# Kernel optimization log

Measured on AMD Instinct MI355X. Metric: run time of the kernel, lower is better.

Reference implementation:

```python
import jax, jax.numpy as jnp
import numpy as np
import math

B, S, D, H, F, L, V = 16, 256, 1024, 16, 4096, 6, 32
HD = D // H
EPS = 1e-6
DIST_DECAY = 0.05  # grid-distance attention decay strength
NEG = -1e9


def _ln(x, w, b):
    mu = jnp.mean(x, axis=-1, keepdims=True)
    var = jnp.mean(jnp.square(x - mu), axis=-1, keepdims=True)
    return (x - mu) * jax.lax.rsqrt(var + EPS) * w + b


def _branch_bias():
    # branch 0: grid-distance decay (distance_matrix = |i-j|)
    # branch 1: register-flow edges i<->i+1 (chain mask)
    # branch 2: entanglement edges on even pairs (2k, 2k+1)
    # branch 3: semantic (full attention, no bias)
    i = jnp.arange(S)
    dist = jnp.abs(i[:, None] - i[None, :]).astype(jnp.float32)  # [S,S]
    reg = dist <= 1.0
    ent = (i[:, None] // 2) == (i[None, :] // 2)
    bias = jnp.stack([
        -DIST_DECAY * dist,
        jnp.where(reg, 0.0, NEG),
        jnp.where(ent, 0.0, NEG),
        jnp.zeros((S, S), jnp.float32),
    ])  # [4,S,S]
    return bias[:, None, None]  # [4,1,1,S,S]


def setup_inputs() -> dict:
    key = jax.random.key(0)
    ks = jax.random.split(key, 20)
    sd = 0.02
    inp = {
        'x': jax.random.normal(ks[0], (B, S, D), jnp.float32),
        't_emb': jax.random.normal(ks[1], (B, D), jnp.float32),
        'ln1_w': jnp.ones((L, D)), 'ln1_b': jnp.zeros((L, D)),
        'ln2_w': jnp.ones((L, D)), 'ln2_b': jnp.zeros((L, D)),
        'Wqkv': jax.random.normal(ks[2], (L, 4, D, 3 * D)) * sd,
        'Wo':   jax.random.normal(ks[3], (L, 4, D, D)) * sd,
        'Wf':   jax.random.normal(ks[4], (L, 4 * D, D)) * sd,
        'bf':   jnp.zeros((L, D)),
        'W1':   jax.random.normal(ks[5], (L, D, F)) * sd,
        'W3':   jax.random.normal(ks[6], (L, D, F)) * sd,
        'W2':   jax.random.normal(ks[7], (L, F, D)) * sd,
        'Wa':   jax.random.normal(ks[8], (L, D, 6 * D)) * sd,
        'ba':   jnp.zeros((L, 6 * D)),
        'fn_w': jnp.ones((D,)), 'fn_b': jnp.zeros((D,)),
        'Wp':   jax.random.normal(ks[9], (D, V)) * sd,
        'bp':   jnp.zeros((V,)),
    }
    return inp


def _quantum_attention(xn, Wqkv_l, Wo_l, Wf_l, bf_l, bias):
    # four attention branches computed in one batched einsum over branch axis x
    qkv = jnp.einsum('bsd,xde->xbse', xn, Wqkv_l)            # [4,B,S,3D]
    qkv = qkv.reshape(4, B, S, 3, H, HD)
    q, k, v = (jnp.moveaxis(qkv[:, :, :, j], 3, 2) for j in range(3))  # [4,B,H,S,HD]
    scores = jnp.einsum('xbhsd,xbhtd->xbhst', q, k) / math.sqrt(HD) + bias
    attn = jax.nn.softmax(scores, axis=-1)
    ctx = jnp.einsum('xbhst,xbhtd->xbhsd', attn, v)          # [4,B,H,S,HD]
    ctx = jnp.moveaxis(ctx, 2, 3).reshape(4, B, S, D)
    outs = jnp.einsum('xbsd,xde->xbse', ctx, Wo_l)           # [4,B,S,D]
    cat = jnp.moveaxis(outs, 0, 2).reshape(B, S, 4 * D)
    return cat @ Wf_l + bf_l                                  # fusion network


def reference(x, t_emb, ln1_w, ln1_b, ln2_w, ln2_b, Wqkv, Wo, Wf, bf, W1, W3, W2, Wa, ba, fn_w, fn_b, Wp, bp):
    bias = _branch_bias()
    for l in range(L):
        # AdaLN timestep conditioning: SiLU -> Linear -> chunk(6)
        a = jax.nn.silu(t_emb) @ Wa[l] + ba[l]
        sh_msa, sc_msa, g_msa, sh_mlp, sc_mlp, g_mlp = jnp.split(a, 6, axis=-1)
        xn = _ln(x, ln1_w[l], ln1_b[l])
        xn = xn * (1.0 + sc_msa[:, None]) + sh_msa[:, None]
        attn_out = _quantum_attention(xn, Wqkv[l], Wo[l], Wf[l], bf[l], bias)
        x = x + g_msa[:, None] * attn_out
        xn = _ln(x, ln2_w[l], ln2_b[l])
        xn = xn * (1.0 + sc_mlp[:, None]) + sh_mlp[:, None]
        ffn = (jax.nn.silu(xn @ W1[l]) * (xn @ W3[l])) @ W2[l]  # SwiGLU
        x = x + g_mlp[:, None] * ffn
    x = _ln(x, fn_w, fn_b)
    return x @ Wp + bp  # noise predictor logits [B,S,V]
```

## Files before the change

kernel.cpp:

```cpp
#include <hip/hip_runtime.h>
#include <hip/hip_bf16.h>
#include <math.h>

#define BB 16
#define SS 256
#define DD 1024
#define HH 16
#define HDD 64
#define FF 4096
#define LL 6
#define VV 32
#define MM (BB*SS)

using bf16 = __hip_bfloat16;
using short8 = __attribute__((ext_vector_type(8))) short;
using f32x4  = __attribute__((ext_vector_type(4))) float;

__device__ __forceinline__ float bf2f(short u){
  unsigned int x = ((unsigned int)(unsigned short)u) << 16;
  return __builtin_bit_cast(float, x);
}
__device__ __forceinline__ short f2bf(float f){
  return __builtin_bit_cast(short, __float2bfloat16(f));
}

__device__ __forceinline__ void gll16(const void* g, void* l) {
  __builtin_amdgcn_global_load_lds(
      (const __attribute__((address_space(1))) void*)g,
      (__attribute__((address_space(3))) void*)l,
      16, 0, 0);
}

__device__ __forceinline__ f32x4 mfma16(short8 a, short8 b, f32x4 c){
  return __builtin_amdgcn_mfma_f32_16x16x32_bf16(a, b, c, 0, 0, 0);
}

__device__ __forceinline__ void st_out(float* p, float v){ *p = v; }
__device__ __forceinline__ void st_out(bf16* p, float v){ *p = __float2bfloat16(v); }

__global__ __launch_bounds__(256)
void tcvt64(const float* __restrict__ in, bf16* __restrict__ out,
            int R, int C, long izs, long ozs)
{
  in  += (long)blockIdx.z * izs;
  out += (long)blockIdx.z * ozs;
  __shared__ float tl[64][65];
  int c0 = blockIdx.x * 64, r0 = blockIdx.y * 64;
  int t = threadIdx.x;
  int tr = t >> 4, tc = (t & 15) * 4;
  #pragma unroll
  for (int i = 0; i < 4; ++i) {
    f32x4 v = *(const f32x4*)(in + (long)(r0 + tr + i*16) * C + c0 + tc);
    tl[tr + i*16][tc+0] = v[0];
    tl[tr + i*16][tc+1] = v[1];
    tl[tr + i*16][tc+2] = v[2];
    tl[tr + i*16][tc+3] = v[3];
  }
  __syncthreads();
  int oc = t >> 2, rch = (t & 3) * 16;
  short8 o0, o1;
  #pragma unroll
  for (int j = 0; j < 8; ++j) o0[j] = f2bf(tl[rch + j][oc]);
  #pragma unroll
  for (int j = 0; j < 8; ++j) o1[j] = f2bf(tl[rch + 8 + j][oc]);
  *(short8*)(out + (long)(c0 + oc) * R + r0 + rch)     = o0;
  *(short8*)(out + (long)(c0 + oc) * R + r0 + rch + 8) = o1;
}

__global__ __launch_bounds__(256)
void cvt(const float* __restrict__ in, bf16* __restrict__ out)
{
  long base = ((long)blockIdx.x * 256 + threadIdx.x) * 8;
  f32x4 a = *(const f32x4*)(in + base);
  f32x4 b = *(const f32x4*)(in + base + 4);
  short8 o;
  #pragma unroll
  for (int j = 0; j < 4; ++j) { o[j] = f2bf(a[j]); o[4+j] = f2bf(b[j]); }
  *(short8*)(out + base) = o;
}

template<typename OUT>
__global__ __launch_bounds__(512, 2)
void gemm256(const bf16* __restrict__ A, const bf16* __restrict__ Bt,
             OUT* __restrict__ C, int K,
             int lda, int ldb, int ldc, int swz)
{
  __shared__ short lds[65536];
  char* L = (char*)lds;
  int lin = blockIdx.x + gridDim.x * blockIdx.y;
  if (swz) {
    int nwg = gridDim.x * gridDim.y;
    int q = nwg >> 3, r = nwg & 7;
    int xcd = lin & 7, o = lin >> 3;
    lin = (xcd < r ? xcd*(q+1) : r*(q+1) + (xcd-r)*q) + o;
  }
  const int n0 = (lin % gridDim.x) * 256;
  const int m0 = (lin / gridDim.x) * 256;
  const int t = threadIdx.x;
  const int wid = t >> 6, lane = t & 63, lo = lane & 15, hi = lane >> 4;
  const int wr = wid >> 2, wc = wid & 3;
  const int rst = t >> 3;
  const int glog = (t & 7) ^ (rst & 7);
  const int wub = wid * 1024;
  const bf16* Ap = A + (long)m0 * lda + glog * 8;
  const bf16* Bp = Bt + (long)n0 * ldb + glog * 8;
  f32x4 acc[8][4] = {};
  const int nkt = K >> 6;

  auto STAGE = [&](int kt, int p, int d) {
    const long ko = (long)kt * 64;
    char* base = L + d*65536;
    if (p < 2) {
      gll16(Ap + (long)((p*2  )*64 + rst)*lda + ko, base + (p*2  )*8192 + wub);
      gll16(Ap + (long)((p*2+1)*64 + rst)*lda + ko, base + (p*2+1)*8192 + wub);
    } else {
      int pp = p - 2;
      gll16(Bp + (long)((pp*2  )*64 + rst)*ldb + ko, base + 32768 + (pp*2  )*8192 + wub);
      gll16(Bp + (long)((pp*2+1)*64 + rst)*ldb + ko, base + 32768 + (pp*2+1)*8192 + wub);
    }
  };

  #pragma unroll
  for (int p = 0; p < 4; ++p) STAGE(0, p, 0);

  short8 af[4][2], b0[2][2], b1[2][2];
  const int gk0 = ((0*4 + hi) ^ (lo & 7)) << 4;
  const int gk1 = ((1*4 + hi) ^ (lo & 7)) << 4;

  for (int kt = 0; kt < nkt; ++kt) {
    const int d = kt & 1;
    const int ktn = (kt+1 < nkt) ? kt+1 : kt;
    char* Ab = L + d*65536;
    char* Bb = Ab + 32768;
    STAGE(ktn, 0, d^1);
    __builtin_amdgcn_sched_barrier(0);
    asm volatile("s_waitcnt vmcnt(2)" ::: "memory");
    __builtin_amdgcn_sched_barrier(0);
    __builtin_amdgcn_s_barrier();
    __builtin_amdgcn_sched_barrier(0);
    #pragma unroll
    for (int mi = 0; mi < 4; ++mi) {
      int r = wr*128 + mi*16 + lo;
      af[mi][0] = *(const short8*)(Ab + r*128 + gk0);
      af[mi][1] = *(const short8*)(Ab + r*128 + gk1);
    }
    #pragma unroll
    for (int ni = 0; ni < 2; ++ni) {
      int r = wc*64 + ni*16 + lo;
      b0[ni][0] = *(const short8*)(Bb + r*128 + gk0);
      b0[ni][1] = *(const short8*)(Bb + r*128 + gk1);
    }
    __builtin_amdgcn_s_barrier();
    __builtin_amdgcn_s_setprio(1);
    #pragma unroll
    for (int mi = 0; mi < 4; ++mi)
      #pragma unroll
      for (int ni = 0; ni < 2; ++ni) {
        acc[mi][ni] = mfma16(af[mi][0], b0[ni][0], acc[mi][ni]);
        acc[mi][ni] = mfma16(af[mi][1], b0[ni][1], acc[mi][ni]);
      }
    __builtin_amdgcn_s_setprio(0);
    __builtin_amdgcn_sched_barrier(0);
    __builtin_amdgcn_s_barrier();
    STAGE(ktn, 1, d^1);
    #pragma unroll
    for (int ni = 0; ni < 2; ++ni) {
      int r = wc*64 + (2+ni)*16 + lo;
      b1[ni][0] = *(const short8*)(Bb + r*128 + gk0);
      b1[ni][1] = *(const short8*)(Bb + r*128 + gk1);
    }
    __builtin_amdgcn_s_barrier();
    __builtin_amdgcn_s_setprio(1);
    #pragma unroll
    for (int mi = 0; mi < 4; ++mi)
      #pragma unroll
      for (int ni = 0; ni < 2; ++ni) {
        acc[mi][2+ni] = mfma16(af[mi][0], b1[ni][0], acc[mi][2+ni]);
        acc[mi][2+ni] = mfma16(af[mi][1], b1[ni][1], acc[mi][2+ni]);
      }
    __builtin_amdgcn_s_setprio(0);
    __builtin_amdgcn_sched_barrier(0);
    __builtin_amdgcn_s_barrier();
    STAGE(ktn, 2, d^1);
    #pragma unroll
    for (int mi = 0; mi < 4; ++mi) {
      int r = wr*128 + (4+mi)*16 + lo;
      af[mi][0] = *(const short8*)(Ab + r*128 + gk0);
      af[mi][1] = *(const short8*)(Ab + r*128 + gk1);
    }
    __builtin_amdgcn_s_barrier();
    __builtin_amdgcn_s_setprio(1);
    #pragma unroll
    for (int mi = 0; mi < 4; ++mi)
      #pragma unroll
      for (int ni = 0; ni < 2; ++ni) {
        acc[4+mi][2+ni] = mfma16(af[mi][0], b1[ni][0], acc[4+mi][2+ni]);
        acc[4+mi][2+ni] = mfma16(af[mi][1], b1[ni][1], acc[4+mi][2+ni]);
      }
    __builtin_amdgcn_s_setprio(0);
    __builtin_amdgcn_sched_barrier(0);
    __builtin_amdgcn_s_barrier();
    STAGE(ktn, 3, d^1);
    __builtin_amdgcn_s_barrier();
    __builtin_amdgcn_s_setprio(1);
    #pragma unroll
    for (int mi = 0; mi < 4; ++mi)
      #pragma unroll
      for (int ni = 0; ni < 2; ++ni) {
        acc[4+mi][ni] = mfma16(af[mi][0], b0[ni][0], acc[4+mi][ni]);
        acc[4+mi][ni] = mfma16(af[mi][1], b0[ni][1], acc[4+mi][ni]);
      }
    __builtin_amdgcn_s_setprio(0);
    __builtin_amdgcn_sched_barrier(0);
    __builtin_amdgcn_s_barrier();
  }
  #pragma unroll
  for (int mi = 0; mi < 8; ++mi)
    #pragma unroll
    for (int ni = 0; ni < 4; ++ni)
      #pragma unroll
      for (int r = 0; r < 4; ++r) {
        int row = m0 + wr*128 + mi*16 + hi*4 + r;
        int col = n0 + wc*64 + ni*16 + lo;
        st_out(C + (long)row * ldc + col, acc[mi][ni][r]);
      }
}

template<typename OUT>
__global__ __launch_bounds__(256)
void gemm_bt(const bf16* __restrict__ A, const bf16* __restrict__ Bt,
             OUT* __restrict__ C, int M, int N, int K,
             int lda, int ldb, int ldc,
             long azs, long bzs, long czs, int swz)
{
  const int z = blockIdx.z;
  A  += (long)z * azs;
  Bt += (long)z * bzs;
  C  += (long)z * czs;
  int bx = blockIdx.x, by = blockIdx.y;
  if (swz) {
    int nwg = gridDim.x * gridDim.y;
    int lin = bx + gridDim.x * by;
    int lin2 = (lin & 7) * (nwg >> 3) + (lin >> 3);
    bx = lin2 % gridDim.x;
    by = lin2 / gridDim.x;
  }
  const int n0 = bx * 128;
  const int m0 = by * 128;
  __shared__ short As[128*64];
  __shared__ short Bs[128*64];
  char* AsB = (char*)As;
  char* BsB = (char*)Bs;
  const int t = threadIdx.x;
  const int wid = t >> 6, lane = t & 63, lo = lane & 15, hi = lane >> 4;
  const int wr = wid >> 1, wc = wid & 1;
  const int rst  = t >> 3;
  const int glog = (t & 7) ^ (rst & 7);
  const int ldsbase = wid * 1024;
  f32x4 acc[4][4] = {};
  const bf16* Ap = A + (long)m0 * lda + glog * 8;
  const bf16* Bp = Bt + (long)n0 * ldb + glog * 8;
  const int nkt = K >> 6;
  for (int kt = 0; kt < nkt; ++kt) {
    const long ko = (long)kt * 64;
    #pragma unroll
    for (int i = 0; i < 4; ++i)
      gll16(Ap + (long)(i*32 + rst) * lda + ko, AsB + i*4096 + ldsbase);
    #pragma unroll
    for (int i = 0; i < 4; ++i)
      gll16(Bp + (long)(i*32 + rst) * ldb + ko, BsB + i*4096 + ldsbase);
    __syncthreads();
    #pragma unroll
    for (int kk = 0; kk < 2; ++kk) {
      const int g = ((kk*4 + hi) ^ (lo & 7)) << 4;
      short8 af[4], bfv[4];
      #pragma unroll
      for (int mi = 0; mi < 4; ++mi) {
        int r = wr*64 + mi*16 + lo;
        af[mi] = *(const short8*)(AsB + r*128 + g);
      }
      #pragma unroll
      for (int ni = 0; ni < 4; ++ni) {
        int r = wc*64 + ni*16 + lo;
        bfv[ni] = *(const short8*)(BsB + r*128 + g);
      }
      #pragma unroll
      for (int mi = 0; mi < 4; ++mi)
        #pragma unroll
        for (int ni = 0; ni < 4; ++ni)
          acc[mi][ni] = mfma16(af[mi], bfv[ni], acc[mi][ni]);
    }
    __syncthreads();
  }
  #pragma unroll
  for (int mi = 0; mi < 4; ++mi)
    #pragma unroll
    for (int ni = 0; ni < 4; ++ni)
      #pragma unroll
      for (int r = 0; r < 4; ++r) {
        int row = m0 + wr*64 + mi*16 + hi*4 + r;
        int col = n0 + wc*64 + ni*16 + lo;
        st_out(C + (long)row * ldc + col, acc[mi][ni][r]);
      }
}

__global__ __launch_bounds__(256)
void vtk(const bf16* __restrict__ qkv, bf16* __restrict__ vt)
{
  int xbh = blockIdx.y;
  int xc = xbh >> 8, b = (xbh >> 4) & 15, h = xbh & 15;
  int x = xc * 3;
  int tch = blockIdx.x;
  const unsigned short* src = (const unsigned short*)qkv
      + (long)(b*SS + tch*64) * 12288 + x*3072 + 2048 + h*64;
  unsigned short* dst = (unsigned short*)vt + (long)xbh * 64 * 256 + tch*64;
  __shared__ unsigned short tl[64][66];
  int t = threadIdx.x;
  #pragma unroll
  for (int i = 0; i < 16; ++i) {
    int idx = t + i*256; int tt = idx >> 6, dd = idx & 63;
    tl[tt][dd] = src[(long)tt * 12288 + dd];
  }
  __syncthreads();
  #pragma unroll
  for (int i = 0; i < 16; ++i) {
    int idx = t + i*256; int dd = idx >> 6, t2 = idx & 63;
    dst[(long)dd * 256 + t2] = tl[t2][dd];
  }
}

__device__ __forceinline__ float bias_f(int x, int i, int j){
  if (x == 0) { int d = i > j ? i - j : j - i; return -0.05f * (float)d; }
  return 0.f;
}

__global__ __launch_bounds__(256)
void attn_k(const bf16* __restrict__ qkv, const bf16* __restrict__ vt,
            bf16* __restrict__ ctx)
{
  const int xc = blockIdx.y;
  const int x = xc * 3;
  const int bh = blockIdx.x;
  const int b = bh >> 4, h = bh & 15;
  const int t = threadIdx.x, wid = t >> 6, lane = t & 63;
  const int lo = lane & 15, hi = lane >> 4;
  const int q0 = wid * 64;
  __shared__ short Pl[4][64*64];
  char* P = (char*)Pl[wid];
  const bf16* qb = qkv + (long)(b*SS) * 12288 + x*3072 + h*64;
  const bf16* kb = qb + 1024;
  const bf16* vb = vt + (long)(xc*256 + b*16 + h) * 64 * 256;

  short8 qf[4][2];
  #pragma unroll
  for (int mi = 0; mi < 4; ++mi)
    #pragma unroll
    for (int kk = 0; kk < 2; ++kk)
      qf[mi][kk] = *(const short8*)(qb + (long)(q0 + mi*16 + lo) * 12288 + kk*32 + hi*8);

  float mr[4][4], sr[4][4];
  f32x4 aco[4][4] = {};
  #pragma unroll
  for (int i = 0; i < 4; ++i)
    #pragma unroll
    for (int r = 0; r < 4; ++r) { mr[i][r] = -INFINITY; sr[i][r] = 0.f; }

  for (int c = 0; c < 4; ++c) {
    f32x4 acc[4][4] = {};
    #pragma unroll
    for (int kk = 0; kk < 2; ++kk) {
      short8 bfv[4];
      #pragma unroll
      for (int ni = 0; ni < 4; ++ni)
        bfv[ni] = *(const short8*)(kb + (long)(c*64 + ni*16 + lo) * 12288 + kk*32 + hi*8);
      #pragma unroll
      for (int mi = 0; mi < 4; ++mi)
        #pragma unroll
        for (int ni = 0; ni < 4; ++ni)
          acc[mi][ni] = mfma16(qf[mi][kk], bfv[ni], acc[mi][ni]);
    }
    float cmax[4][4];
    #pragma unroll
    for (int mi = 0; mi < 4; ++mi)
      #pragma unroll
      for (int r = 0; r < 4; ++r) cmax[mi][r] = -INFINITY;
    #pragma unroll
    for (int mi = 0; mi < 4; ++mi)
      #pragma unroll
      for (int ni = 0; ni < 4; ++ni)
        #pragma unroll
        for (int r = 0; r < 4; ++r) {
          int qq = q0 + mi*16 + hi*4 + r;
          int tt = c*64 + ni*16 + lo;
          float v = acc[mi][ni][r] * 0.125f + bias_f(x, qq, tt);
          acc[mi][ni][r] = v;
          cmax[mi][r] = fmaxf(cmax[mi][r], v);
        }
    #pragma unroll
    for (int mi = 0; mi < 4; ++mi)
      #pragma unroll
      for (int r = 0; r < 4; ++r) {
        float m = cmax[mi][r];
        #pragma unroll
        for (int d = 1; d < 16; d <<= 1) m = fmaxf(m, __shfl_xor(m, d));
        cmax[mi][r] = m;
      }
    float fs[4][4];
    #pragma unroll
    for (int mi = 0; mi < 4; ++mi)
      #pragma unroll
      for (int r = 0; r < 4; ++r) {
        float mo = mr[mi][r];
        float mn = fmaxf(mo, cmax[mi][r]);
        float f = __expf(mo - mn);
        mr[mi][r] = mn; sr[mi][r] *= f; fs[mi][r] = f;
      }
    #pragma unroll
    for (int mi = 0; mi < 4; ++mi)
      #pragma unroll
      for (int di = 0; di < 4; ++di)
        #pragma unroll
        for (int r = 0; r < 4; ++r) aco[mi][di][r] *= fs[mi][r];
    #pragma unroll
    for (int mi = 0; mi < 4; ++mi)
      #pragma unroll
      for (int ni = 0; ni < 4; ++ni)
        #pragma unroll
        for (int r = 0; r < 4; ++r) {
          int qq = mi*16 + hi*4 + r;
          float pv = __expf(acc[mi][ni][r] - mr[mi][r]);
          sr[mi][r] += pv;
          int tt = ni*16 + lo;
          int gph = ((tt >> 3) ^ (qq & 7)) << 4;
          *(bf16*)(P + qq*128 + gph + (tt & 7)*2) = __float2bfloat16(pv);
        }
    #pragma unroll
    for (int kk = 0; kk < 2; ++kk) {
      short8 pf[4], vf[4];
      #pragma unroll
      for (int mi = 0; mi < 4; ++mi) {
        int qq = mi*16 + lo;
        int gph = ((kk*4 + hi) ^ (qq & 7)) << 4;
        pf[mi] = *(const short8*)(P + qq*128 + gph);
      }
      #pragma unroll
      for (int di = 0; di < 4; ++di)
        vf[di] = *(const short8*)(vb + (long)(di*16 + lo) * 256 + c*64 + kk*32 + hi*8);
      #pragma unroll
      for (int mi = 0; mi < 4; ++mi)
        #pragma unroll
        for (int di = 0; di < 4; ++di)
          aco[mi][di] = mfma16(pf[mi], vf[di], aco[mi][di]);
    }
  }
  #pragma unroll
  for (int mi = 0; mi < 4; ++mi)
    #pragma unroll
    for (int r = 0; r < 4; ++r) {
      float s = sr[mi][r];
      #pragma unroll
      for (int d = 1; d < 16; d <<= 1) s += __shfl_xor(s, d);
      sr[mi][r] = s;
    }
  bf16* cb = ctx + (long)(b*SS) * 4096 + x*1024 + h*64;
  #pragma unroll
  for (int mi = 0; mi < 4; ++mi)
    #pragma unroll
    for (int di = 0; di < 4; ++di)
      #pragma unroll
      for (int r = 0; r < 4; ++r) {
        int row = q0 + mi*16 + hi*4 + r;
        int col = di*16 + lo;
        cb[(long)row * 4096 + col] = __float2bfloat16(aco[mi][di][r] / sr[mi][r]);
      }
}

__global__ __launch_bounds__(256)
void br12_k(const bf16* __restrict__ qkv, bf16* __restrict__ ctx)
{
  const unsigned short* Q = (const unsigned short*)qkv;
  const int wid = threadIdx.x >> 6, lane = threadIdx.x & 63;
  const int b = blockIdx.x >> 6, c = blockIdx.x & 63;
  const int i = c*4 + wid;
  const long rowQ = (long)(b*SS + i) * 12288;
  const long rb = (long)(b*SS) * 12288;
  const int jm = i > 0 ? i-1 : 0;
  const int jp = i < SS-1 ? i+1 : SS-1;
  const int j0 = i & ~1, j1 = j0 | 1;
  unsigned short* outp = (unsigned short*)ctx + (long)(b*SS + i) * 4096;
  for (int h = 0; h < HH; ++h) {
    const int off1 = 3072 + h*64 + lane;
    const int off2 = 6144 + h*64 + lane;
    float q1d = bf2f(Q[rowQ + off1]);
    float q2d = bf2f(Q[rowQ + off2]);
    float km = bf2f(Q[rb + (long)jm*12288 + off1 + 1024]);
    float k0 = bf2f(Q[rb + (long)i *12288 + off1 + 1024]);
    float kp = bf2f(Q[rb + (long)jp*12288 + off1 + 1024]);
    float ka = bf2f(Q[rb + (long)j0*12288 + off2 + 1024]);
    float kb_ = bf2f(Q[rb + (long)j1*12288 + off2 + 1024]);
    float s0 = q1d*km, s1 = q1d*k0, s2 = q1d*kp, s3 = q2d*ka, s4 = q2d*kb_;
    #pragma unroll
    for (int st = 1; st < 64; st <<= 1) {
      s0 += __shfl_xor(s0, st); s1 += __shfl_xor(s1, st); s2 += __shfl_xor(s2, st);
      s3 += __shfl_xor(s3, st); s4 += __shfl_xor(s4, st);
    }
    float lm = s0*0.125f + (i > 0      ? 0.f : -1e30f);
    float l0 = s1*0.125f;
    float lp = s2*0.125f + (i < SS-1   ? 0.f : -1e30f);
    float m1 = fmaxf(l0, fmaxf(lm, lp));
    float pm = __expf(lm-m1), p0 = __expf(l0-m1), pp = __expf(lp-m1);
    float vm = bf2f(Q[rb + (long)jm*12288 + off1 + 2048]);
    float v0 = bf2f(Q[rb + (long)i *12288 + off1 + 2048]);
    float vp = bf2f(Q[rb + (long)jp*12288 + off1 + 2048]);
    float o1 = (pm*vm + p0*v0 + pp*vp) / (pm+p0+pp);
    float la = s3*0.125f, lb = s4*0.125f;
    float m2 = fmaxf(la, lb);
    float pa = __expf(la-m2), pb = __expf(lb-m2);
    float va = bf2f(Q[rb + (long)j0*12288 + off2 + 2048]);
    float vb2= bf2f(Q[rb + (long)j1*12288 + off2 + 2048]);
    float o2 = (pa*va + pb*vb2) / (pa+pb);
    outp[1024 + h*64 + lane] = (unsigned short)f2bf(o1);
    outp[2048 + h*64 + lane] = (unsigned short)f2bf(o2);
  }
}

__global__ __launch_bounds__(256)
void swiglu_k(const bf16* __restrict__ h, bf16* __restrict__ g)
{
  long base = ((long)blockIdx.x * 256 + threadIdx.x) * 8;
  long s = base >> 12, n = base & 4095;
  const short8 a = *(const short8*)(h + s*8192 + n);
  const short8 b = *(const short8*)(h + s*8192 + 4096 + n);
  short8 o;
  #pragma unroll
  for (int j = 0; j < 8; ++j) {
    float av = bf2f(a[j]), bv = bf2f(b[j]);
    float sv = av / (1.f + __expf(-av)) * bv;
    o[j] = f2bf(sv);
  }
  *(short8*)(g + s*4096 + n) = o;
}

__global__ __launch_bounds__(256)
void ln_fused(const float* __restrict__ xin, const float* __restrict__ y,
              const float* __restrict__ y2,
              const float* __restrict__ ybias, const float* __restrict__ gate,
              const float* __restrict__ lnw, const float* __restrict__ lnb,
              const float* __restrict__ sc, const float* __restrict__ sh,
              float* __restrict__ xout, bf16* __restrict__ xnbf,
              float* __restrict__ xnf)
{
  int row = blockIdx.x;
  int b = row >> 8;
  int t = threadIdx.x;
  int d0 = t * 4;
  const float* xr = xin + (long)row * DD;
  f32x4 xi = *(const f32x4*)(xr + d0);
  float v[4];
  if (y) {
    f32x4 yi = *(const f32x4*)(y + (long)row * DD + d0);
    f32x4 y2i = {};
    if (y2) y2i = *(const f32x4*)(y2 + (long)row * DD + d0);
    #pragma unroll
    for (int j = 0; j < 4; ++j) {
      float yy = yi[j] + y2i[j] + (ybias ? ybias[d0+j] : 0.f);
      v[j] = xi[j] + gate[b*6144 + d0 + j] * yy;
    }
  } else {
    #pragma unroll
    for (int j = 0; j < 4; ++j) v[j] = xi[j];
  }
  if (xout) {
    f32x4 o; o[0]=v[0]; o[1]=v[1]; o[2]=v[2]; o[3]=v[3];
    *(f32x4*)(xout + (long)row * DD + d0) = o;
  }
  float s = v[0]+v[1]+v[2]+v[3];
  float s2 = v[0]*v[0]+v[1]*v[1]+v[2]*v[2]+v[3]*v[3];
  #pragma unroll
  for (int d = 1; d < 64; d <<= 1) { s += __shfl_xor(s, d); s2 += __shfl_xor(s2, d); }
  __shared__ float rs[4][2];
  int wid = t >> 6, lane = t & 63;
  if (lane == 0) { rs[wid][0] = s; rs[wid][1] = s2; }
  __syncthreads();
  s  = rs[0][0]+rs[1][0]+rs[2][0]+rs[3][0];
  s2 = rs[0][1]+rs[1][1]+rs[2][1]+rs[3][1];
  float mean = s * (1.f/1024.f);
  float var  = s2 * (1.f/1024.f) - mean*mean;
  float rstd = rsqrtf(var + 1e-6f);
  #pragma unroll
  for (int j = 0; j < 4; ++j) {
    int d = d0 + j;
    float xn = (v[j] - mean) * rstd * lnw[d] + lnb[d];
    if (sc) {
      float val = xn * (1.f + sc[b*6144 + d]) + sh[b*6144 + d];
      xnbf[(long)row * DD + d] = __float2bfloat16(val);
    } else if (xnbf) {
      xnbf[(long)row * DD + d] = __float2bfloat16(xn);
    } else {
      xnf[(long)row * DD + d] = xn;
    }
  }
}

__global__ __launch_bounds__(256)
void silu_k(const float* __restrict__ te, float* __restrict__ st)
{
  int i = blockIdx.x * 256 + threadIdx.x;
  float v = te[i];
  st[i] = v / (1.f + __expf(-v));
}

__global__ __launch_bounds__(256)
void a_gemm(const float* __restrict__ Wa, const float* __restrict__ st,
            float* __restrict__ partial)
{
  int l = blockIdx.z, kc = blockIdx.y;
  int n = blockIdx.x * 256 + threadIdx.x;
  __shared__ float sl[16*256];
  for (int i = threadIdx.x; i < 16*256; i += 256) {
    int m = i >> 8, k = i & 255;
    sl[i] = st[m*1024 + kc*256 + k];
  }
  __syncthreads();
  float acc[16] = {};
  const float* wp = Wa + (long)l * DD * 6144 + (long)(kc*256) * 6144 + n;
  #pragma unroll 4
  for (int k = 0; k < 256; ++k) {
    float w = wp[(long)k * 6144];
    #pragma unroll
    for (int m = 0; m < 16; ++m) acc[m] += sl[m*256 + k] * w;
  }
  #pragma unroll
  for (int m = 0; m < 16; ++m)
    partial[((long)(l*4 + kc)*16 + m) * 6144 + n] = acc[m];
}

__global__ __launch_bounds__(256)
void a_red(const float* __restrict__ partial, const float* __restrict__ ba,
           float* __restrict__ a_all)
{
  int idx = blockIdx.x * 256 + threadIdx.x;
  int n = idx % 6144;
  int lm = idx / 6144;
  int l = lm >> 4, m = lm & 15;
  float s = 0.f;
  #pragma unroll
  for (int kc = 0; kc < 4; ++kc)
    s += partial[((long)(l*4 + kc)*16 + m) * 6144 + n];
  a_all[(long)(l*16 + m) * 6144 + n] = s + ba[(long)l * 6144 + n];
}

__global__ __launch_bounds__(256)
void proj_k(const float* __restrict__ xnf, const float* __restrict__ Wp,
            const float* __restrict__ bp, float* __restrict__ out)
{
  int v = threadIdx.x & 31, tg = threadIdx.x >> 5;
  int s = blockIdx.x * 8 + tg;
  const float* xr = xnf + (long)s * DD;
  float acc = bp[v];
  #pragma unroll 8
  for (int k = 0; k < DD; ++k) acc += xr[k] * Wp[(long)k * VV + v];
  out[(long)s * VV + v] = acc;
}

extern "C" void kernel_launch(void* const* d_in, const int* in_sizes, int n_in,
                              void* d_out, int out_size, void* d_ws, size_t ws_size,
                              hipStream_t stream)
{
  (void)in_sizes; (void)n_in; (void)out_size; (void)ws_size;
  const float* x_in = (const float*)d_in[0];
  const float* t_emb= (const float*)d_in[1];
  const float* ln1w = (const float*)d_in[2];
  const float* ln1b = (const float*)d_in[3];
  const float* ln2w = (const float*)d_in[4];
  const float* ln2b = (const float*)d_in[5];
  const float* Wqkv = (const float*)d_in[6];
  const float* Wo   = (const float*)d_in[7];
  const float* Wf   = (const float*)d_in[8];
  const float* bfb  = (const float*)d_in[9];
  const float* W1   = (const float*)d_in[10];
  const float* W3   = (const float*)d_in[11];
  const float* W2   = (const float*)d_in[12];
  const float* Wa   = (const float*)d_in[13];
  const float* ba   = (const float*)d_in[14];
  const float* fnw  = (const float*)d_in[15];
  const float* fnb  = (const float*)d_in[16];
  const float* Wp   = (const float*)d_in[17];
  const float* bp   = (const float*)d_in[18];
  float* out = (float*)d_out;

  char* p = (char*)d_ws;
  auto alloc = [&](size_t bytes) { char* r = p; p += (bytes + 255) & ~(size_t)255; return r; };
  bf16* wqkv_t = (bf16*)alloc(4L*3072*1024*2);
  bf16* wo_b   = (bf16*)alloc(4L*1024*1024*2);
  bf16* wf_t   = (bf16*)alloc(1024L*4096*2);
  bf16* wof_t  = (bf16*)alloc(1024L*4096*2);
  bf16* w13_t  = (bf16*)alloc(8192L*1024*2);
  bf16* w2_t   = (bf16*)alloc(1024L*4096*2);
  float* a_all = (float*)alloc(6L*16*6144*4);
  float* a_par = (float*)alloc(6L*4*16*6144*4);
  float* st    = (float*)alloc(16L*1024*4);
  float* x_buf = (float*)alloc((long)MM*DD*4);
  bf16* xn     = (bf16*)alloc((long)MM*DD*2);
  char* bufA   = alloc((long)MM*12288*2);
  bf16* vt     = (bf16*)alloc(2L*16*16*64*256*2);
  bf16* ctx    = (bf16*)alloc((long)MM*4096*2);
  char* bufB   = alloc((long)MM*4096*2);
  float* gy    = (float*)alloc(2L*MM*DD*4);

  bf16* qkvb = (bf16*)bufA;
  bf16* h13  = (bf16*)bufA;
  bf16* hg   = (bf16*)bufB;
  float* xnf = (float*)bufB;
  float* gy2 = gy + (long)MM*DD;

  silu_k<<<dim3(64), 256, 0, stream>>>(t_emb, st);
  a_gemm<<<dim3(24, 4, 6), 256, 0, stream>>>(Wa, st, a_par);
  a_red<<<dim3(2304), 256, 0, stream>>>(a_par, ba, a_all);

  const long aL = 16L * 6144;
  for (int l = 0; l < LL; ++l) {
    const float* a_l = a_all + (long)l * aL;
    tcvt64<<<dim3(48,16,4),256,0,stream>>>(Wqkv + (long)l*4*1024*3072, wqkv_t, 1024, 3072, 1024L*3072, 3072L*1024);
    cvt<<<dim3(2048),256,0,stream>>>(Wo + (long)l*4*1024*1024, wo_b);
    tcvt64<<<dim3(16,64,1),256,0,stream>>>(Wf  + (long)l*4096*1024,  wf_t,   4096, 1024, 0, 0);
    tcvt64<<<dim3(64,16,1),256,0,stream>>>(W1  + (long)l*1024*4096,  w13_t,  1024, 4096, 0, 0);
    tcvt64<<<dim3(64,16,1),256,0,stream>>>(W3  + (long)l*1024*4096,  w13_t + 4096L*1024, 1024, 4096, 0, 0);
    tcvt64<<<dim3(16,64,1),256,0,stream>>>(W2  + (long)l*4096*1024,  w2_t,   4096, 1024, 0, 0);
    gemm_bt<bf16><<<dim3(8,8,4),256,0,stream>>>(wf_t, wo_b, wof_t,
        1024, 1024, 1024, 4096, 1024, 4096, 1024L, 1024L*1024, 1024L, 0);

    if (l == 0)
      ln_fused<<<4096,256,0,stream>>>(x_in, nullptr, nullptr, nullptr, nullptr,
                                      ln1w, ln1b, a_l+1024, a_l+0,
                                      nullptr, xn, nullptr);

    gemm256<bf16><<<dim3(48,16),512,0,stream>>>(xn, wqkv_t, qkvb, 1024, 1024, 1024, 12288, 1);
    vtk<<<dim3(4,512),256,0,stream>>>(qkvb, vt);
    attn_k<<<dim3(256,2),256,0,stream>>>(qkvb, vt, ctx);
    br12_k<<<dim3(1024),256,0,stream>>>(qkvb, ctx);
    gemm_bt<float><<<dim3(8,32,2),256,0,stream>>>(ctx, wof_t, gy,
        MM, 1024, 2048, 4096, 4096, 1024, 2048L, 2048L, (long)MM*DD, 0);
    ln_fused<<<4096,256,0,stream>>>(l ? x_buf : x_in, gy, gy2, bfb + (long)l*1024, a_l+2048,
                                    ln2w + (long)l*1024, ln2b + (long)l*1024,
                                    a_l+4096, a_l+3072, x_buf, xn, nullptr);
    gemm256<bf16><<<dim3(32,16),512,0,stream>>>(xn, w13_t, h13, 1024, 1024, 1024, 8192, 1);
    swiglu_k<<<dim3(8192),256,0,stream>>>(h13, hg);
    gemm_bt<float><<<dim3(8,32,2),256,0,stream>>>(hg, w2_t, gy,
        MM, 1024, 2048, 4096, 4096, 1024, 2048L, 2048L, (long)MM*DD, 0);
    if (l < LL-1)
      ln_fused<<<4096,256,0,stream>>>(x_buf, gy, gy2, nullptr, a_l+5120,
                                      ln1w + (long)(l+1)*1024, ln1b + (long)(l+1)*1024,
                                      a_all + (long)(l+1)*aL + 1024, a_all + (long)(l+1)*aL,
                                      x_buf, xn, nullptr);
    else
      ln_fused<<<4096,256,0,stream>>>(x_buf, gy, gy2, nullptr, a_l+5120,
                                      fnw, fnb, nullptr, nullptr,
                                      x_buf, nullptr, xnf);
  }
  proj_k<<<dim3(512),256,0,stream>>>(xnf, Wp, bp, out);
}
```

Before: 3.198 ms.

## Fuse SwiGLU into W1/W3 GEMM epilogue and use split-K gemm256 for down projections

```diff
diff --git a/kernel.cpp b/kernel.cpp
--- a/kernel.cpp
+++ b/kernel.cpp
@@ -68,6 +68,37 @@
 }
 
 __global__ __launch_bounds__(256)
+void tcvt64_w13(const float* __restrict__ W1, const float* __restrict__ W3,
+                bf16* __restrict__ out, long loff)
+{
+  const float* in = (blockIdx.z ? W3 : W1) + loff;
+  const int zoff = blockIdx.z ? 16 : 0;
+  __shared__ float tl[64][65];
+  int c0 = blockIdx.x * 64, r0 = blockIdx.y * 64;
+  int t = threadIdx.x;
+  int tr = t >> 4, tc = (t & 15) * 4;
+  #pragma unroll
+  for (int i = 0; i < 4; ++i) {
+    f32x4 v = *(const f32x4*)(in + (long)(r0 + tr + i*16) * 4096 + c0 + tc);
+    tl[tr + i*16][tc+0] = v[0];
+    tl[tr + i*16][tc+1] = v[1];
+    tl[tr + i*16][tc+2] = v[2];
+    tl[tr + i*16][tc+3] = v[3];
+  }
+  __syncthreads();
+  int oc = t >> 2, rch = (t & 3) * 16;
+  short8 o0, o1;
+  #pragma unroll
+  for (int j = 0; j < 8; ++j) o0[j] = f2bf(tl[rch + j][oc]);
+  #pragma unroll
+  for (int j = 0; j < 8; ++j) o1[j] = f2bf(tl[rch + 8 + j][oc]);
+  int n = c0 + oc;
+  int orow = ((n >> 4) << 5) + zoff + (n & 15);
+  *(short8*)(out + (long)orow * 1024 + r0 + rch)     = o0;
+  *(short8*)(out + (long)orow * 1024 + r0 + rch + 8) = o1;
+}
+
+__global__ __launch_bounds__(256)
 void cvt(const float* __restrict__ in, bf16* __restrict__ out)
 {
   long base = ((long)blockIdx.x * 256 + threadIdx.x) * 8;
@@ -79,14 +110,17 @@
   *(short8*)(out + base) = o;
 }
 
-template<typename OUT>
+template<typename OUT, int MODE>
 __global__ __launch_bounds__(512, 2)
 void gemm256(const bf16* __restrict__ A, const bf16* __restrict__ Bt,
              OUT* __restrict__ C, int K,
-             int lda, int ldb, int ldc, int swz)
+             int lda, int ldb, int ldc, long kzs, long czs, int swz)
 {
   __shared__ short lds[65536];
   char* L = (char*)lds;
+  A  += (long)blockIdx.z * kzs;
+  Bt += (long)blockIdx.z * kzs;
+  C  += (long)blockIdx.z * czs;
   int lin = blockIdx.x + gridDim.x * blockIdx.y;
   if (swz) {
     int nwg = gridDim.x * gridDim.y;
@@ -214,16 +248,31 @@
     __builtin_amdgcn_sched_barrier(0);
     __builtin_amdgcn_s_barrier();
   }
-  #pragma unroll
-  for (int mi = 0; mi < 8; ++mi)
-    #pragma unroll
-    for (int ni = 0; ni < 4; ++ni)
-      #pragma unroll
-      for (int r = 0; r < 4; ++r) {
-        int row = m0 + wr*128 + mi*16 + hi*4 + r;
-        int col = n0 + wc*64 + ni*16 + lo;
-        st_out(C + (long)row * ldc + col, acc[mi][ni][r]);
-      }
+  if (MODE == 0) {
+    #pragma unroll
+    for (int mi = 0; mi < 8; ++mi)
+      #pragma unroll
+      for (int ni = 0; ni < 4; ++ni)
+        #pragma unroll
+        for (int r = 0; r < 4; ++r) {
+          int row = m0 + wr*128 + mi*16 + hi*4 + r;
+          int col = n0 + wc*64 + ni*16 + lo;
+          st_out(C + (long)row * ldc + col, acc[mi][ni][r]);
+        }
+  } else {
+    #pragma unroll
+    for (int mi = 0; mi < 8; ++mi)
+      #pragma unroll
+      for (int k = 0; k < 2; ++k)
+        #pragma unroll
+        for (int r = 0; r < 4; ++r) {
+          float h1 = acc[mi][2*k][r], h3 = acc[mi][2*k+1][r];
+          float sv = h1 / (1.f + __expf(-h1)) * h3;
+          int row = m0 + wr*128 + mi*16 + hi*4 + r;
+          int col = (n0 >> 1) + wc*32 + k*16 + lo;
+          st_out(C + (long)row * ldc + col, sv);
+        }
+  }
 }
 
 template<typename OUT>
@@ -525,25 +574,8 @@
 }
 
 __global__ __launch_bounds__(256)
-void swiglu_k(const bf16* __restrict__ h, bf16* __restrict__ g)
-{
-  long base = ((long)blockIdx.x * 256 + threadIdx.x) * 8;
-  long s = base >> 12, n = base & 4095;
-  const short8 a = *(const short8*)(h + s*8192 + n);
-  const short8 b = *(const short8*)(h + s*8192 + 4096 + n);
-  short8 o;
-  #pragma unroll
-  for (int j = 0; j < 8; ++j) {
-    float av = bf2f(a[j]), bv = bf2f(b[j]);
-    float sv = av / (1.f + __expf(-av)) * bv;
-    o[j] = f2bf(sv);
-  }
-  *(short8*)(g + s*4096 + n) = o;
-}
-
-__global__ __launch_bounds__(256)
 void ln_fused(const float* __restrict__ xin, const float* __restrict__ y,
-              const float* __restrict__ y2,
+              int ycnt, long ystride,
               const float* __restrict__ ybias, const float* __restrict__ gate,
               const float* __restrict__ lnw, const float* __restrict__ lnb,
               const float* __restrict__ sc, const float* __restrict__ sh,
@@ -558,12 +590,15 @@
   f32x4 xi = *(const f32x4*)(xr + d0);
   float v[4];
   if (y) {
-    f32x4 yi = *(const f32x4*)(y + (long)row * DD + d0);
-    f32x4 y2i = {};
-    if (y2) y2i = *(const f32x4*)(y2 + (long)row * DD + d0);
+    f32x4 ys = {};
+    for (int jp = 0; jp < ycnt; ++jp) {
+      f32x4 yi = *(const f32x4*)(y + jp*ystride + (long)row * DD + d0);
+      #pragma unroll
+      for (int j = 0; j < 4; ++j) ys[j] += yi[j];
+    }
     #pragma unroll
     for (int j = 0; j < 4; ++j) {
-      float yy = yi[j] + y2i[j] + (ybias ? ybias[d0+j] : 0.f);
+      float yy = ys[j] + (ybias ? ybias[d0+j] : 0.f);
       v[j] = xi[j] + gate[b*6144 + d0 + j] * yy;
     }
   } else {
@@ -615,24 +650,28 @@
             float* __restrict__ partial)
 {
   int l = blockIdx.z, kc = blockIdx.y;
-  int n = blockIdx.x * 256 + threadIdx.x;
-  __shared__ float sl[16*256];
-  for (int i = threadIdx.x; i < 16*256; i += 256) {
-    int m = i >> 8, k = i & 255;
-    sl[i] = st[m*1024 + kc*256 + k];
+  int n0 = (blockIdx.x * 256 + threadIdx.x) * 4;
+  __shared__ float sl[16*128];
+  for (int i = threadIdx.x; i < 16*128; i += 256) {
+    int m = i >> 7, k = i & 127;
+    sl[i] = st[m*1024 + kc*128 + k];
   }
   __syncthreads();
-  float acc[16] = {};
-  const float* wp = Wa + (long)l * DD * 6144 + (long)(kc*256) * 6144 + n;
-  #pragma unroll 4
-  for (int k = 0; k < 256; ++k) {
-    float w = wp[(long)k * 6144];
-    #pragma unroll
-    for (int m = 0; m < 16; ++m) acc[m] += sl[m*256 + k] * w;
+  f32x4 acc[16] = {};
+  const float* wp = Wa + (long)l * DD * 6144 + (long)(kc*128) * 6144 + n0;
+  #pragma unroll 2
+  for (int k = 0; k < 128; ++k) {
+    f32x4 w = *(const f32x4*)(wp + (long)k * 6144);
+    #pragma unroll
+    for (int m = 0; m < 16; ++m) {
+      float sv = sl[m*128 + k];
+      #pragma unroll
+      for (int j = 0; j < 4; ++j) acc[m][j] += sv * w[j];
+    }
   }
   #pragma unroll
   for (int m = 0; m < 16; ++m)
-    partial[((long)(l*4 + kc)*16 + m) * 6144 + n] = acc[m];
+    *(f32x4*)(partial + ((long)(l*8 + kc)*16 + m) * 6144 + n0) = acc[m];
 }
 
 __global__ __launch_bounds__(256)
@@ -645,8 +684,8 @@
   int l = lm >> 4, m = lm & 15;
   float s = 0.f;
   #pragma unroll
-  for (int kc = 0; kc < 4; ++kc)
-    s += partial[((long)(l*4 + kc)*16 + m) * 6144 + n];
+  for (int kc = 0; kc < 8; ++kc)
+    s += partial[((long)(l*8 + kc)*16 + m) * 6144 + n];
   a_all[(long)(l*16 + m) * 6144 + n] = s + ba[(long)l * 6144 + n];
 }
 
@@ -695,10 +734,10 @@
   bf16* wo_b   = (bf16*)alloc(4L*1024*1024*2);
   bf16* wf_t   = (bf16*)alloc(1024L*4096*2);
   bf16* wof_t  = (bf16*)alloc(1024L*4096*2);
-  bf16* w13_t  = (bf16*)alloc(8192L*1024*2);
+  bf16* w13i_t = (bf16*)alloc(8192L*1024*2);
   bf16* w2_t   = (bf16*)alloc(1024L*4096*2);
   float* a_all = (float*)alloc(6L*16*6144*4);
-  float* a_par = (float*)alloc(6L*4*16*6144*4);
+  float* a_par = (float*)alloc(6L*8*16*6144*4);
   float* st    = (float*)alloc(16L*1024*4);
   float* x_buf = (float*)alloc((long)MM*DD*4);
   bf16* xn     = (bf16*)alloc((long)MM*DD*2);
@@ -706,16 +745,15 @@
   bf16* vt     = (bf16*)alloc(2L*16*16*64*256*2);
   bf16* ctx    = (bf16*)alloc((long)MM*4096*2);
   char* bufB   = alloc((long)MM*4096*2);
-  float* gy    = (float*)alloc(2L*MM*DD*4);
+  float* gy    = (float*)alloc(4L*MM*DD*4);
 
   bf16* qkvb = (bf16*)bufA;
-  bf16* h13  = (bf16*)bufA;
   bf16* hg   = (bf16*)bufB;
   float* xnf = (float*)bufB;
-  float* gy2 = gy + (long)MM*DD;
+  const long MMDD = (long)MM*DD;
 
   silu_k<<<dim3(64), 256, 0, stream>>>(t_emb, st);
-  a_gemm<<<dim3(24, 4, 6), 256, 0, stream>>>(Wa, st, a_par);
+  a_gemm<<<dim3(6, 8, 6), 256, 0, stream>>>(Wa, st, a_par);
   a_red<<<dim3(2304), 256, 0, stream>>>(a_par, ba, a_all);
 
   const long aL = 16L * 6144;
@@ -724,37 +762,38 @@
     tcvt64<<<dim3(48,16,4),256,0,stream>>>(Wqkv + (long)l*4*1024*3072, wqkv_t, 1024, 3072, 1024L*3072, 3072L*1024);
     cvt<<<dim3(2048),256,0,stream>>>(Wo + (long)l*4*1024*1024, wo_b);
     tcvt64<<<dim3(16,64,1),256,0,stream>>>(Wf  + (long)l*4096*1024,  wf_t,   4096, 1024, 0, 0);
-    tcvt64<<<dim3(64,16,1),256,0,stream>>>(W1  + (long)l*1024*4096,  w13_t,  1024, 4096, 0, 0);
-    tcvt64<<<dim3(64,16,1),256,0,stream>>>(W3  + (long)l*1024*4096,  w13_t + 4096L*1024, 1024, 4096, 0, 0);
+    tcvt64_w13<<<dim3(64,16,2),256,0,stream>>>(W1, W3, w13i_t, (long)l*1024*4096);
     tcvt64<<<dim3(16,64,1),256,0,stream>>>(W2  + (long)l*4096*1024,  w2_t,   4096, 1024, 0, 0);
     gemm_bt<bf16><<<dim3(8,8,4),256,0,stream>>>(wf_t, wo_b, wof_t,
         1024, 1024, 1024, 4096, 1024, 4096, 1024L, 1024L*1024, 1024L, 0);
 
     if (l == 0)
-      ln_fused<<<4096,256,0,stream>>>(x_in, nullptr, nullptr, nullptr, nullptr,
+      ln_fused<<<4096,256,0,stream>>>(x_in, nullptr, 0, 0, nullptr, nullptr,
                                       ln1w, ln1b, a_l+1024, a_l+0,
                                       nullptr, xn, nullptr);
 
-    gemm256<bf16><<<dim3(48,16),512,0,stream>>>(xn, wqkv_t, qkvb, 1024, 1024, 1024, 12288, 1);
+    gemm256<bf16,0><<<dim3(48,16,1),512,0,stream>>>(xn, wqkv_t, qkvb,
+        1024, 1024, 1024, 12288, 0, 0, 1);
     vtk<<<dim3(4,512),256,0,stream>>>(qkvb, vt);
     attn_k<<<dim3(256,2),256,0,stream>>>(qkvb, vt, ctx);
     br12_k<<<dim3(1024),256,0,stream>>>(qkvb, ctx);
-    gemm_bt<float><<<dim3(8,32,2),256,0,stream>>>(ctx, wof_t, gy,
-        MM, 1024, 2048, 4096, 4096, 1024, 2048L, 2048L, (long)MM*DD, 0);
-    ln_fused<<<4096,256,0,stream>>>(l ? x_buf : x_in, gy, gy2, bfb + (long)l*1024, a_l+2048,
+    gemm256<float,0><<<dim3(4,16,4),512,0,stream>>>(ctx, wof_t, gy,
+        1024, 4096, 4096, 1024, 1024L, MMDD, 0);
+    ln_fused<<<4096,256,0,stream>>>(l ? x_buf : x_in, gy, 4, MMDD,
+                                    bfb + (long)l*1024, a_l+2048,
                                     ln2w + (long)l*1024, ln2b + (long)l*1024,
                                     a_l+4096, a_l+3072, x_buf, xn, nullptr);
-    gemm256<bf16><<<dim3(32,16),512,0,stream>>>(xn, w13_t, h13, 1024, 1024, 1024, 8192, 1);
-    swiglu_k<<<dim3(8192),256,0,stream>>>(h13, hg);
-    gemm_bt<float><<<dim3(8,32,2),256,0,stream>>>(hg, w2_t, gy,
-        MM, 1024, 2048, 4096, 4096, 1024, 2048L, 2048L, (long)MM*DD, 0);
+    gemm256<bf16,1><<<dim3(32,16,1),512,0,stream>>>(xn, w13i_t, hg,
+        1024, 1024, 1024, 4096, 0, 0, 1);
+    gemm256<float,0><<<dim3(4,16,4),512,0,stream>>>(hg, w2_t, gy,
+        1024, 4096, 4096, 1024, 1024L, MMDD, 0);
     if (l < LL-1)
-      ln_fused<<<4096,256,0,stream>>>(x_buf, gy, gy2, nullptr, a_l+5120,
+      ln_fused<<<4096,256,0,stream>>>(x_buf, gy, 4, MMDD, nullptr, a_l+5120,
                                       ln1w + (long)(l+1)*1024, ln1b + (long)(l+1)*1024,
                                       a_all + (long)(l+1)*aL + 1024, a_all + (long)(l+1)*aL,
                                       x_buf, xn, nullptr);
     else
-      ln_fused<<<4096,256,0,stream>>>(x_buf, gy, gy2, nullptr, a_l+5120,
+      ln_fused<<<4096,256,0,stream>>>(x_buf, gy, 4, MMDD, nullptr, a_l+5120,
                                       fnw, fnb, nullptr, nullptr,
                                       x_buf, nullptr, xnf);
   }
```

Measured after the change: 3.009 ms. 1.06x faster.
